# Performance work log

Hardware: AMD Instinct MI355X
Metric: run time of the kernel (lower is better)

Reference implementation:

```python
import jax, jax.numpy as jnp
import numpy as np

B = 32768      # batch
S = 512        # state_dim
G = 128        # goal_dim
A = 32         # action_dim
P = 16         # num_primitives
H1, H2 = 512, 256        # big_model hidden sizes
VH1, VH2 = 1024, 512     # value hidden sizes


def _w(k, shape, scale=0.05):
    return jax.random.normal(k, shape, jnp.float32) * scale


def setup_inputs() -> dict:
    key = jax.random.key(0)
    ks = jax.random.split(key, 24)
    d = {"features": jax.random.normal(ks[0], (B, S + G), jnp.float32)}
    # state encoder: S->H1->H2
    d["se_w1"] = _w(ks[1], (S, H1));  d["se_b1"] = jnp.zeros((H1,), jnp.float32)
    d["se_w2"] = _w(ks[2], (H1, H2)); d["se_b2"] = jnp.zeros((H2,), jnp.float32)
    # goal encoder: G->H1->H2
    d["ge_w1"] = _w(ks[3], (G, H1));  d["ge_b1"] = jnp.zeros((H1,), jnp.float32)
    d["ge_w2"] = _w(ks[4], (H1, H2)); d["ge_b2"] = jnp.zeros((H2,), jnp.float32)
    # gate: 2*H2->H2->P (sigmoid)
    d["gt_w1"] = _w(ks[5], (2 * H2, H2)); d["gt_b1"] = jnp.zeros((H2,), jnp.float32)
    d["gt_w2"] = _w(ks[6], (H2, P));      d["gt_b2"] = jnp.zeros((P,), jnp.float32)
    # primitive state encoder: S->H1->H2
    d["pse_w1"] = _w(ks[7], (S, H1));  d["pse_b1"] = jnp.zeros((H1,), jnp.float32)
    d["pse_w2"] = _w(ks[8], (H1, H2)); d["pse_b2"] = jnp.zeros((H2,), jnp.float32)
    # P primitives, each H2->H2->2A (stacked for batched GEMM)
    d["pw1"] = _w(ks[9], (P, H2, H2));     d["pb1"] = jnp.zeros((P, H2), jnp.float32)
    d["pw2"] = _w(ks[10], (P, H2, 2 * A)); d["pb2"] = jnp.zeros((P, 2 * A), jnp.float32)
    # value net: (S+G)->VH1->VH2
    d["vf_w1"] = _w(ks[11], (S + G, VH1)); d["vf_b1"] = jnp.zeros((VH1,), jnp.float32)
    d["vf_w2"] = _w(ks[12], (VH1, VH2));   d["vf_b2"] = jnp.zeros((VH2,), jnp.float32)
    return d


def _mlp2(x, w1, b1, w2, b2):
    return jax.nn.relu(jax.nn.relu(x @ w1 + b1) @ w2 + b2)


def reference(features,
              se_w1, se_b1, se_w2, se_b2,
              ge_w1, ge_b1, ge_w2, ge_b2,
              gt_w1, gt_b1, gt_w2, gt_b2,
              pse_w1, pse_b1, pse_w2, pse_b2,
              pw1, pb1, pw2, pb2,
              vf_w1, vf_b1, vf_w2, vf_b2):
    state, goal = features[:, :S], features[:, S:]
    # gating weights
    s_emb = _mlp2(state, se_w1, se_b1, se_w2, se_b2)      # [B,H2]
    g_emb = _mlp2(goal, ge_w1, ge_b1, ge_w2, ge_b2)       # [B,H2]
    gate_in = jnp.concatenate([s_emb, g_emb], axis=-1)    # [B,2*H2]
    weights = jax.nn.sigmoid(jax.nn.relu(gate_in @ gt_w1 + gt_b1) @ gt_w2 + gt_b2)  # [B,P]
    # shared primitive embedding
    prim_embed = _mlp2(state, pse_w1, pse_b1, pse_w2, pse_b2)  # [B,H2]
    # all primitives as one batched GEMM
    h = jax.nn.relu(jnp.einsum('bh,phk->bpk', prim_embed, pw1) + pb1[None])  # [B,P,H2]
    out = jnp.einsum('bpk,pkd->bpd', h, pw2) + pb2[None]                      # [B,P,2A]
    mu, log_std = out[..., :A], out[..., A:]
    sigma = jnp.exp(log_std)
    # precision-weighted Gaussian mixture
    inv = weights[..., None] / sigma        # [B,P,A]
    denom = inv.sum(axis=1)                 # [B,A]
    mean = (inv * mu).sum(axis=1) / denom   # [B,A]  (learn_log_std=True -> mean only)
    # critic
    value = _mlp2(features, vf_w1, vf_b1, vf_w2, vf_b2)  # [B,VH2]
    return (mean, value)
```

## Files before the change

kernel.cpp:

```cpp
#include <hip/hip_runtime.h>
#include <stdint.h>

#define NB 32768

typedef __bf16 bf16x8 __attribute__((ext_vector_type(8)));
typedef float f32x4 __attribute__((ext_vector_type(4)));

__device__ __forceinline__ unsigned short f2bf(float f) {
  union { float f; unsigned u; } v; v.f = f;
  unsigned r = v.u + 0x7fffu + ((v.u >> 16) & 1u);
  return (unsigned short)(r >> 16);
}
__device__ __forceinline__ float bf2f(unsigned short h) {
  union { unsigned u; float f; } v; v.u = ((unsigned)h) << 16;
  return v.f;
}

__device__ __forceinline__ void gld_lds16(void* lds, const void* g) {
  __builtin_amdgcn_global_load_lds(
      (__attribute__((address_space(1))) unsigned int*)(uintptr_t)g,
      (__attribute__((address_space(3))) unsigned int*)(uintptr_t)lds,
      16, 0, 0);
}


__global__ __launch_bounds__(256) void fconv_k(const float* __restrict__ src,
                                               unsigned short* __restrict__ dst) {
  size_t idx = ((size_t)blockIdx.x * 256 + threadIdx.x) * 8;
  float4 a = *(const float4*)(src + idx);
  float4 b = *(const float4*)(src + idx + 4);
  union { unsigned short us[8]; uint4 v; } u;
  u.us[0] = f2bf(a.x); u.us[1] = f2bf(a.y); u.us[2] = f2bf(a.z); u.us[3] = f2bf(a.w);
  u.us[4] = f2bf(b.x); u.us[5] = f2bf(b.y); u.us[6] = f2bf(b.z); u.us[7] = f2bf(b.w);
  *(uint4*)(dst + idx) = u.v;
}

struct TJobs {
  const float* src[11];
  unsigned short* dst[11];
  int K[11], N[11], batch[11];
};

__global__ __launch_bounds__(256) void wtrans_k(TJobs jobs) {
  const int job = blockIdx.y;
  const int K = jobs.K[job], N = jobs.N[job];
  const int KT = K >> 5, NT = N >> 5;
  const int ntiles = jobs.batch[job] * KT * NT;
  const int t = blockIdx.x;
  if (t >= ntiles) return;
  const int b = t / (KT * NT);
  const int rem = t - b * KT * NT;
  const int kt = rem / NT, nt = rem - kt * NT;
  const float* src = jobs.src[job] + (size_t)b * K * N;
  unsigned short* dst = jobs.dst[job] + (size_t)b * K * N;
  __shared__ float tile[32][33];
  const int i = threadIdx.x >> 5, jj = threadIdx.x & 31;
#pragma unroll
  for (int s = 0; s < 4; ++s)
    tile[i + 8 * s][jj] = src[(size_t)(kt * 32 + i + 8 * s) * N + nt * 32 + jj];
  __syncthreads();
#pragma unroll
  for (int s = 0; s < 4; ++s)
    dst[(size_t)(nt * 32 + i + 8 * s) * K + kt * 32 + jj] = f2bf(tile[jj][i + 8 * s]);
}


template <bool OUT_BF16>
__global__ __launch_bounds__(256) void gemm_k(const unsigned short* __restrict__ A, int lda,
                                              const unsigned short* __restrict__ WT,
                                              const float* __restrict__ bias,
                                              void* __restrict__ Cout, int ldc, int K) {
  __shared__ unsigned short lds_a[128 * 32];
  __shared__ unsigned short lds_b[128 * 32];
  const int tid = threadIdx.x;
  const int l = tid & 63, w = tid >> 6;
  const int wm = w >> 1, wn = w & 1;
  const int lr = l & 15, lq = l >> 4;
  const int row0 = blockIdx.x << 7;
  const int col0 = blockIdx.y << 7;
  const int srow = tid >> 2;
  const int scg = tid & 3;
  const int wbase = tid & ~63;

  f32x4 acc[4][4] = {};

  for (int k0 = 0; k0 < K; k0 += 32) {
#pragma unroll
    for (int i = 0; i < 2; ++i) {
      const int r = i * 64 + srow;
      gld_lds16(&lds_a[(size_t)(i * 256 + wbase) * 8],
                A + (size_t)(row0 + r) * lda + k0 + scg * 8);
      gld_lds16(&lds_b[(size_t)(i * 256 + wbase) * 8],
                WT + (size_t)(col0 + r) * K + k0 + scg * 8);
    }
    __syncthreads();
    bf16x8 av[4], bv[4];
#pragma unroll
    for (int mf = 0; mf < 4; ++mf)
      av[mf] = *(const bf16x8*)&lds_a[((wm * 64 + mf * 16 + lr) << 5) + (lq << 3)];
#pragma unroll
    for (int nf = 0; nf < 4; ++nf)
      bv[nf] = *(const bf16x8*)&lds_b[((wn * 64 + nf * 16 + lr) << 5) + (lq << 3)];
#pragma unroll
    for (int mf = 0; mf < 4; ++mf)
#pragma unroll
      for (int nf = 0; nf < 4; ++nf)
        acc[mf][nf] = __builtin_amdgcn_mfma_f32_16x16x32_bf16(av[mf], bv[nf], acc[mf][nf], 0, 0, 0);
    __syncthreads();
  }

#pragma unroll
  for (int nf = 0; nf < 4; ++nf) {
    const int gc = col0 + wn * 64 + nf * 16 + lr;
    const float bb = bias[gc];
#pragma unroll
    for (int mf = 0; mf < 4; ++mf) {
      const int gr = row0 + wm * 64 + mf * 16 + (lq << 2);
#pragma unroll
      for (int r = 0; r < 4; ++r) {
        float v = acc[mf][nf][r] + bb;
        v = fmaxf(v, 0.0f);
        if (OUT_BF16)
          ((unsigned short*)Cout)[(size_t)(gr + r) * ldc + gc] = f2bf(v);
        else
          ((float*)Cout)[(size_t)(gr + r) * ldc + gc] = v;
      }
    }
  }
}


template <bool OUT_BF16>
__global__ __launch_bounds__(256, 2) void gemm2_k(const unsigned short* __restrict__ A, int lda,
                                                  const unsigned short* __restrict__ WT,
                                                  const float* __restrict__ bias,
                                                  void* __restrict__ Cout, int ldc, int K) {
  __shared__ unsigned short a_s[2][128 * 32];
  __shared__ unsigned short b_s[2][256 * 32];
  const int tid = threadIdx.x;
  const int l = tid & 63, w = tid >> 6;
  const int lr = l & 15, lq = l >> 4;
  const int row0 = blockIdx.x << 7;
  const int col0 = blockIdx.y << 8;
  const int wbase = tid & ~63;

  auto stage = [&](int buf, int t) {
    const int k0 = t << 5;
#pragma unroll
    for (int i = 0; i < 2; ++i) {
      const int s = i * 256 + tid;
      const int r = s >> 2, c = s & 3;
      const int cs = c ^ ((r >> 1) & 3);
      gld_lds16(&a_s[buf][(size_t)(i * 256 + wbase) * 8],
                A + (size_t)(row0 + r) * lda + k0 + cs * 8);
    }
#pragma unroll
    for (int i = 0; i < 4; ++i) {
      const int s = i * 256 + tid;
      const int n = s >> 2, c = s & 3;
      const int cs = c ^ ((n >> 1) & 3);
      gld_lds16(&b_s[buf][(size_t)(i * 256 + wbase) * 8],
                WT + (size_t)(col0 + n) * K + k0 + cs * 8);
    }
  };

  f32x4 acc[8][4] = {};
  const int nt = K >> 5;
  stage(0, 0);
  __syncthreads();
#pragma unroll 1
  for (int t = 0; t < nt; ++t) {
    const int cur = t & 1;
    if (t + 1 < nt) stage(cur ^ 1, t + 1);
    bf16x8 av[8], bv[4];
#pragma unroll
    for (int mf = 0; mf < 8; ++mf) {
      const int r = mf * 16 + lr;
      av[mf] = *(const bf16x8*)&a_s[cur][r * 32 + ((lq ^ ((r >> 1) & 3)) << 3)];
    }
#pragma unroll
    for (int nf = 0; nf < 4; ++nf) {
      const int n = w * 64 + nf * 16 + lr;
      bv[nf] = *(const bf16x8*)&b_s[cur][n * 32 + ((lq ^ ((n >> 1) & 3)) << 3)];
    }
#pragma unroll
    for (int mf = 0; mf < 8; ++mf)
#pragma unroll
      for (int nf = 0; nf < 4; ++nf)
        acc[mf][nf] = __builtin_amdgcn_mfma_f32_16x16x32_bf16(av[mf], bv[nf], acc[mf][nf], 0, 0, 0);
    __syncthreads();
  }

#pragma unroll
  for (int nf = 0; nf < 4; ++nf) {
    const int gc = col0 + w * 64 + nf * 16 + lr;
    const float bb = bias[gc];
#pragma unroll
    for (int mf = 0; mf < 8; ++mf) {
      const int gr = row0 + mf * 16 + (lq << 2);
#pragma unroll
      for (int r = 0; r < 4; ++r) {
        float v = acc[mf][nf][r] + bb;
        v = fmaxf(v, 0.0f);
        if (OUT_BF16)
          ((unsigned short*)Cout)[(size_t)(gr + r) * ldc + gc] = f2bf(v);
        else
          ((float*)Cout)[(size_t)(gr + r) * ldc + gc] = v;
      }
    }
  }
}


__global__ __launch_bounds__(256) void gt2_k(const unsigned short* __restrict__ gate_h,
                                             const float* __restrict__ w2,
                                             const float* __restrict__ b2,
                                             float* __restrict__ wgt) {
  __shared__ float w_s[256 * 16];
  __shared__ unsigned short a_s[16 * 264];
  const int tid = threadIdx.x;
  const int row0 = blockIdx.x * 16;
  for (int i = tid; i < 256 * 16; i += 256) w_s[i] = w2[i];
  for (int i = tid; i < 512; i += 256) {
    const int r = i >> 5, cg = i & 31;
    *(uint4*)&a_s[r * 264 + cg * 8] =
        *(const uint4*)(gate_h + (size_t)(row0 + r) * 256 + cg * 8);
  }
  __syncthreads();
  const int rr = tid >> 4, col = tid & 15;
  float sum = b2[col];
#pragma unroll 8
  for (int k = 0; k < 256; ++k)
    sum += bf2f(a_s[rr * 264 + k]) * w_s[k * 16 + col];
  wgt[(size_t)(row0 + rr) * 16 + col] = 1.0f / (1.0f + __expf(-sum));
}


__global__ __launch_bounds__(512, 4) void prim_head_k(
    const unsigned short* __restrict__ prim,
    const float* __restrict__ wgt,
    const unsigned short* __restrict__ pw1t,
    const float* __restrict__ pb1,
    const unsigned short* __restrict__ pw2t,
    const float* __restrict__ pb2,
    unsigned short* __restrict__ outbuf)
{
  __shared__ unsigned short prim_s[2][128 * 32];
  __shared__ unsigned short w1_s[2][128 * 32];
  __shared__ unsigned short h_s[128 * 128];
  __shared__ unsigned short pw2_s[64 * 128];
  const int tid = threadIdx.x;
  const int l = tid & 63;
  const int w = tid >> 6;
  const int lr = l & 15, lq = l >> 4;
  const int wn2 = w & 1, wr2 = w >> 1;
  const int row0 = blockIdx.x << 7;
  const int p = blockIdx.y;
  const int wbase = tid & ~63;

  const unsigned short* w1p = pw1t + (size_t)p * 65536;
  const unsigned short* w2p = pw2t + (size_t)p * 16384;

  auto stage_ab = [&](int t) {
    const int buf = t & 1;
    const int k0 = (t & 7) << 5;
    const int nb2 = (t >> 3) << 7;
    const int rw = tid >> 2, kc = tid & 3;
    const int kcs = kc ^ ((rw >> 1) & 3);
    gld_lds16(&prim_s[buf][(size_t)wbase * 8],
              prim + (size_t)(row0 + rw) * 256 + k0 + kcs * 8);
    gld_lds16(&w1_s[buf][(size_t)wbase * 8],
              w1p + (size_t)(nb2 + rw) * 256 + k0 + kcs * 8);
  };
  auto stage_pw2 = [&](int half) {
    const int nbase = half << 7;
#pragma unroll
    for (int i = 0; i < 2; ++i) {
      const int c = i * 512 + tid;
      const int d = c >> 4, kc = c & 15;
      gld_lds16(&pw2_s[(size_t)(i * 512 + wbase) * 8],
                w2p + (size_t)d * 256 + nbase + ((kc ^ (d & 7)) << 3));
    }
  };

  stage_ab(0);
  stage_pw2(0);
  __syncthreads();

  f32x4 acc2[2][2] = {};

  for (int half = 0; half < 2; ++half) {
    float4 pb1v[4];
#pragma unroll
    for (int nf = 0; nf < 4; ++nf)
      pb1v[nf] = *(const float4*)(pb1 + p * 256 + (half << 7) + wn2 * 64 + nf * 16 + (lq << 2));

    f32x4 acc1[4][2] = {};
#pragma unroll 1
    for (int ks = 0; ks < 8; ++ks) {
      const int t = (half << 3) + ks;
      const int cur = t & 1;
      if (t < 15) stage_ab(t + 1);
      bf16x8 av[4], bv[2];
#pragma unroll
      for (int nf = 0; nf < 4; ++nf) {
        const int n = wn2 * 64 + nf * 16 + lr;
        av[nf] = *(const bf16x8*)&w1_s[cur][n * 32 + ((lq ^ ((n >> 1) & 3)) << 3)];
      }
#pragma unroll
      for (int rf = 0; rf < 2; ++rf) {
        const int r = wr2 * 32 + rf * 16 + lr;
        bv[rf] = *(const bf16x8*)&prim_s[cur][r * 32 + ((lq ^ ((r >> 1) & 3)) << 3)];
      }
#pragma unroll
      for (int nf = 0; nf < 4; ++nf)
#pragma unroll
        for (int rf = 0; rf < 2; ++rf)
          acc1[nf][rf] = __builtin_amdgcn_mfma_f32_16x16x32_bf16(av[nf], bv[rf], acc1[nf][rf], 0, 0, 0);
      __syncthreads();
    }

#pragma unroll
    for (int nf = 0; nf < 4; ++nf) {
      const int n0 = wn2 * 64 + nf * 16 + (lq << 2);
      const float4 bb = pb1v[nf];
#pragma unroll
      for (int rf = 0; rf < 2; ++rf) {
        const int row = wr2 * 32 + rf * 16 + lr;
        const float v0 = fmaxf(acc1[nf][rf][0] + bb.x, 0.0f);
        const float v1 = fmaxf(acc1[nf][rf][1] + bb.y, 0.0f);
        const float v2 = fmaxf(acc1[nf][rf][2] + bb.z, 0.0f);
        const float v3 = fmaxf(acc1[nf][rf][3] + bb.w, 0.0f);
        uint2 pk;
        pk.x = (unsigned)f2bf(v0) | ((unsigned)f2bf(v1) << 16);
        pk.y = (unsigned)f2bf(v2) | ((unsigned)f2bf(v3) << 16);
        *(uint2*)&h_s[row * 128 + (((n0 >> 3) ^ (row & 7)) << 3) + (n0 & 7)] = pk;
      }
    }
    __syncthreads();

    {
      const int dmu = wn2 * 16;
      const int row_a = wr2 * 32;
#pragma unroll
      for (int kc8 = 0; kc8 < 4; ++kc8) {
        const int slot = ((kc8 << 2) + lq) ^ (lr & 7);
        const bf16x8 amu = *(const bf16x8*)&pw2_s[(dmu + lr) * 128 + (slot << 3)];
        const bf16x8 als = *(const bf16x8*)&pw2_s[(dmu + 32 + lr) * 128 + (slot << 3)];
        const bf16x8 b0 = *(const bf16x8*)&h_s[(row_a + lr) * 128 + (slot << 3)];
        const bf16x8 b1 = *(const bf16x8*)&h_s[(row_a + 16 + lr) * 128 + (slot << 3)];
        acc2[0][0] = __builtin_amdgcn_mfma_f32_16x16x32_bf16(amu, b0, acc2[0][0], 0, 0, 0);
        acc2[0][1] = __builtin_amdgcn_mfma_f32_16x16x32_bf16(als, b0, acc2[0][1], 0, 0, 0);
        acc2[1][0] = __builtin_amdgcn_mfma_f32_16x16x32_bf16(amu, b1, acc2[1][0], 0, 0, 0);
        acc2[1][1] = __builtin_amdgcn_mfma_f32_16x16x32_bf16(als, b1, acc2[1][1], 0, 0, 0);
      }
    }
    __syncthreads();
    if (half == 0) stage_pw2(1);
  }

  {
    const int dmu = wn2 * 16;
    const int row_a = wr2 * 32;
    const int d0 = dmu + (lq << 2);
    const float4 b2mu = *(const float4*)(pb2 + p * 64 + d0);
    const float4 b2ls = *(const float4*)(pb2 + p * 64 + 32 + d0);
    const float wp0 = wgt[(size_t)(row0 + row_a + lr) * 16 + p];
    const float wp1 = wgt[(size_t)(row0 + row_a + 16 + lr) * 16 + p];
#pragma unroll
    for (int s = 0; s < 2; ++s) {
      const int row_g = row0 + row_a + s * 16 + lr;
      const float wp = s ? wp1 : wp0;
      unsigned short* ob = outbuf + ((size_t)row_g * 16 + p) * 64;
      const float mu0 = acc2[s][0][0] + b2mu.x, ls0 = acc2[s][1][0] + b2ls.x;
      const float mu1 = acc2[s][0][1] + b2mu.y, ls1 = acc2[s][1][1] + b2ls.y;
      const float mu2 = acc2[s][0][2] + b2mu.z, ls2 = acc2[s][1][2] + b2ls.z;
      const float mu3 = acc2[s][0][3] + b2mu.w, ls3 = acc2[s][1][3] + b2ls.w;
      const float iv0 = wp * __expf(-ls0), iv1 = wp * __expf(-ls1);
      const float iv2 = wp * __expf(-ls2), iv3 = wp * __expf(-ls3);
      uint2 nmp, ivp;
      nmp.x = (unsigned)f2bf(iv0 * mu0) | ((unsigned)f2bf(iv1 * mu1) << 16);
      nmp.y = (unsigned)f2bf(iv2 * mu2) | ((unsigned)f2bf(iv3 * mu3) << 16);
      ivp.x = (unsigned)f2bf(iv0) | ((unsigned)f2bf(iv1) << 16);
      ivp.y = (unsigned)f2bf(iv2) | ((unsigned)f2bf(iv3) << 16);
      *(uint2*)(ob + d0) = nmp;
      *(uint2*)(ob + 32 + d0) = ivp;
    }
  }
}


__global__ __launch_bounds__(256) void mix_finish_k(const unsigned short* __restrict__ buf,
                                                    float* __restrict__ mean_out) {
  const int gid = blockIdx.x * 256 + threadIdx.x;
  const int row = gid >> 3;
  const int a0 = (gid & 7) * 4;
  const unsigned short* rp = buf + (size_t)row * 1024;
  float nx = 0, ny = 0, nz = 0, nw = 0, dx = 0, dy = 0, dz = 0, dw = 0;
#pragma unroll
  for (int p = 0; p < 16; ++p) {
    const uint2 m = *(const uint2*)(rp + p * 64 + a0);
    const uint2 v = *(const uint2*)(rp + p * 64 + 32 + a0);
    nx += bf2f((unsigned short)(m.x & 0xffff)); ny += bf2f((unsigned short)(m.x >> 16));
    nz += bf2f((unsigned short)(m.y & 0xffff)); nw += bf2f((unsigned short)(m.y >> 16));
    dx += bf2f((unsigned short)(v.x & 0xffff)); dy += bf2f((unsigned short)(v.x >> 16));
    dz += bf2f((unsigned short)(v.y & 0xffff)); dw += bf2f((unsigned short)(v.y >> 16));
  }
  float4 res;
  res.x = nx / dx; res.y = ny / dy; res.z = nz / dz; res.w = nw / dw;
  *(float4*)(mean_out + (size_t)row * 32 + a0) = res;
}


extern "C" void kernel_launch(void* const* d_in, const int* in_sizes, int n_in,
                              void* d_out, int out_size, void* d_ws, size_t ws_size,
                              hipStream_t stream) {
  const float* features = (const float*)d_in[0];
  const float* se_w1 = (const float*)d_in[1];
  const float* se_b1 = (const float*)d_in[2];
  const float* se_w2 = (const float*)d_in[3];
  const float* se_b2 = (const float*)d_in[4];
  const float* ge_w1 = (const float*)d_in[5];
  const float* ge_b1 = (const float*)d_in[6];
  const float* ge_w2 = (const float*)d_in[7];
  const float* ge_b2 = (const float*)d_in[8];
  const float* gt_w1 = (const float*)d_in[9];
  const float* gt_b1 = (const float*)d_in[10];
  const float* gt_w2 = (const float*)d_in[11];
  const float* gt_b2 = (const float*)d_in[12];
  const float* pse_w1 = (const float*)d_in[13];
  const float* pse_b1 = (const float*)d_in[14];
  const float* pse_w2 = (const float*)d_in[15];
  const float* pse_b2 = (const float*)d_in[16];
  const float* pw1 = (const float*)d_in[17];
  const float* pb1 = (const float*)d_in[18];
  const float* pw2 = (const float*)d_in[19];
  const float* pb2 = (const float*)d_in[20];
  const float* vf_w1 = (const float*)d_in[21];
  const float* vf_b1 = (const float*)d_in[22];
  const float* vf_w2 = (const float*)d_in[23];
  const float* vf_b2 = (const float*)d_in[24];
  (void)in_sizes; (void)n_in; (void)out_size; (void)ws_size;

  char* base = (char*)d_ws;
  size_t off = 0;
  auto alloc = [&](size_t bytes) -> char* {
    char* p = base + off;
    off += (bytes + 255) & ~(size_t)255;
    return p;
  };
  unsigned short* fbf     = (unsigned short*)alloc((size_t)NB * 640 * 2);
  unsigned short* bufA    = (unsigned short*)alloc((size_t)NB * 1024 * 2);
  unsigned short* g1      = (unsigned short*)alloc((size_t)NB * 512 * 2);
  unsigned short* gate_in = (unsigned short*)alloc((size_t)NB * 512 * 2);
  unsigned short* gate_h  = (unsigned short*)alloc((size_t)NB * 256 * 2);
  unsigned short* prim    = (unsigned short*)alloc((size_t)NB * 256 * 2);
  float* wgt              = (float*)alloc((size_t)NB * 16 * 4);
  unsigned short* se_w1t  = (unsigned short*)alloc(512 * 512 * 2);
  unsigned short* se_w2t  = (unsigned short*)alloc(256 * 512 * 2);
  unsigned short* ge_w1t  = (unsigned short*)alloc(512 * 128 * 2);
  unsigned short* ge_w2t  = (unsigned short*)alloc(256 * 512 * 2);
  unsigned short* gt_w1t  = (unsigned short*)alloc(256 * 512 * 2);
  unsigned short* pse_w1t = (unsigned short*)alloc(512 * 512 * 2);
  unsigned short* pse_w2t = (unsigned short*)alloc(256 * 512 * 2);
  unsigned short* pw1t    = (unsigned short*)alloc((size_t)16 * 256 * 256 * 2);
  unsigned short* pw2t    = (unsigned short*)alloc((size_t)16 * 64 * 256 * 2);
  unsigned short* vf_w1t  = (unsigned short*)alloc(1024 * 640 * 2);
  unsigned short* vf_w2t  = (unsigned short*)alloc(512 * 1024 * 2);

  unsigned short* outbuf = (unsigned short*)bufA;

  float* mean_out = (float*)d_out;
  float* value_out = (float*)d_out + (size_t)NB * 32;

  fconv_k<<<dim3(10240), dim3(256), 0, stream>>>(features, fbf);

  TJobs jobs;
  auto setj = [&](int i, const float* s, unsigned short* d, int K, int N, int b) {
    jobs.src[i] = s; jobs.dst[i] = d; jobs.K[i] = K; jobs.N[i] = N; jobs.batch[i] = b;
  };
  setj(0, se_w1, se_w1t, 512, 512, 1);
  setj(1, se_w2, se_w2t, 512, 256, 1);
  setj(2, ge_w1, ge_w1t, 128, 512, 1);
  setj(3, ge_w2, ge_w2t, 512, 256, 1);
  setj(4, gt_w1, gt_w1t, 512, 256, 1);
  setj(5, pse_w1, pse_w1t, 512, 512, 1);
  setj(6, pse_w2, pse_w2t, 512, 256, 1);
  setj(7, pw1, pw1t, 256, 256, 16);
  setj(8, pw2, pw2t, 256, 64, 16);
  setj(9, vf_w1, vf_w1t, 640, 1024, 1);
  setj(10, vf_w2, vf_w2t, 1024, 512, 1);
  wtrans_k<<<dim3(1024, 11), dim3(256), 0, stream>>>(jobs);

  gemm2_k<true><<<dim3(256, 2), dim3(256), 0, stream>>>(fbf, 640, se_w1t, se_b1, bufA, 512, 512);
  gemm_k<true><<<dim3(256, 2), dim3(256), 0, stream>>>(bufA, 512, se_w2t, se_b2, gate_in, 512, 512);
  gemm2_k<true><<<dim3(256, 2), dim3(256), 0, stream>>>(fbf + 512, 640, ge_w1t, ge_b1, g1, 512, 128);
  gemm_k<true><<<dim3(256, 2), dim3(256), 0, stream>>>(g1, 512, ge_w2t, ge_b2, gate_in + 256, 512, 512);
  gemm_k<true><<<dim3(256, 2), dim3(256), 0, stream>>>(gate_in, 512, gt_w1t, gt_b1, gate_h, 256, 512);
  gt2_k<<<dim3(2048), dim3(256), 0, stream>>>(gate_h, gt_w2, gt_b2, wgt);
  gemm2_k<true><<<dim3(256, 2), dim3(256), 0, stream>>>(fbf, 640, pse_w1t, pse_b1, bufA, 512, 512);
  gemm_k<true><<<dim3(256, 2), dim3(256), 0, stream>>>(bufA, 512, pse_w2t, pse_b2, prim, 256, 512);
  gemm2_k<true><<<dim3(256, 4), dim3(256), 0, stream>>>(fbf, 640, vf_w1t, vf_b1, bufA, 1024, 640);
  gemm2_k<false><<<dim3(256, 2), dim3(256), 0, stream>>>(bufA, 1024, vf_w2t, vf_b2, value_out, 512, 1024);
  prim_head_k<<<dim3(256, 16), dim3(512), 0, stream>>>(prim, wgt, pw1t, pb1, pw2t, pb2, outbuf);
  mix_finish_k<<<dim3(1024), dim3(256), 0, stream>>>(outbuf, mean_out);
}
```

Before: 478.8 us.

## Replace single-buffered GEMM with double-buffered swizzled kernel and XCD-aware tile mapping

Replaces the old single-buffered 128x128 gemm_k with a new gemm3_k. The new kernel double-buffers its LDS tiles so the next K-slice loads while the current one computes, and uses an XOR swizzle to reduce LDS bank conflicts. Both GEMM kernels now take a 1D grid and remap block ids so consecutive tiles land on the same XCD, which improves L2 reuse of A rows across column tiles. The cost is more LDS per block and extra index arithmetic, and the grid sizes must stay divisible by 8.

```diff
diff --git a/kernel.cpp b/kernel.cpp
--- a/kernel.cpp
+++ b/kernel.cpp
@@ -21,6 +21,10 @@
       (__attribute__((address_space(1))) unsigned int*)(uintptr_t)g,
       (__attribute__((address_space(3))) unsigned int*)(uintptr_t)lds,
       16, 0, 0);
+}
+
+__device__ __forceinline__ int xcd_swz(int bid, int nwg) {
+  return (bid & 7) * (nwg >> 3) + (bid >> 3);
 }
 
 
@@ -66,82 +70,19 @@
 
 
 template <bool OUT_BF16>
-__global__ __launch_bounds__(256) void gemm_k(const unsigned short* __restrict__ A, int lda,
-                                              const unsigned short* __restrict__ WT,
-                                              const float* __restrict__ bias,
-                                              void* __restrict__ Cout, int ldc, int K) {
-  __shared__ unsigned short lds_a[128 * 32];
-  __shared__ unsigned short lds_b[128 * 32];
-  const int tid = threadIdx.x;
-  const int l = tid & 63, w = tid >> 6;
-  const int wm = w >> 1, wn = w & 1;
-  const int lr = l & 15, lq = l >> 4;
-  const int row0 = blockIdx.x << 7;
-  const int col0 = blockIdx.y << 7;
-  const int srow = tid >> 2;
-  const int scg = tid & 3;
-  const int wbase = tid & ~63;
-
-  f32x4 acc[4][4] = {};
-
-  for (int k0 = 0; k0 < K; k0 += 32) {
-#pragma unroll
-    for (int i = 0; i < 2; ++i) {
-      const int r = i * 64 + srow;
-      gld_lds16(&lds_a[(size_t)(i * 256 + wbase) * 8],
-                A + (size_t)(row0 + r) * lda + k0 + scg * 8);
-      gld_lds16(&lds_b[(size_t)(i * 256 + wbase) * 8],
-                WT + (size_t)(col0 + r) * K + k0 + scg * 8);
-    }
-    __syncthreads();
-    bf16x8 av[4], bv[4];
-#pragma unroll
-    for (int mf = 0; mf < 4; ++mf)
-      av[mf] = *(const bf16x8*)&lds_a[((wm * 64 + mf * 16 + lr) << 5) + (lq << 3)];
-#pragma unroll
-    for (int nf = 0; nf < 4; ++nf)
-      bv[nf] = *(const bf16x8*)&lds_b[((wn * 64 + nf * 16 + lr) << 5) + (lq << 3)];
-#pragma unroll
-    for (int mf = 0; mf < 4; ++mf)
-#pragma unroll
-      for (int nf = 0; nf < 4; ++nf)
-        acc[mf][nf] = __builtin_amdgcn_mfma_f32_16x16x32_bf16(av[mf], bv[nf], acc[mf][nf], 0, 0, 0);
-    __syncthreads();
-  }
-
-#pragma unroll
-  for (int nf = 0; nf < 4; ++nf) {
-    const int gc = col0 + wn * 64 + nf * 16 + lr;
-    const float bb = bias[gc];
-#pragma unroll
-    for (int mf = 0; mf < 4; ++mf) {
-      const int gr = row0 + wm * 64 + mf * 16 + (lq << 2);
-#pragma unroll
-      for (int r = 0; r < 4; ++r) {
-        float v = acc[mf][nf][r] + bb;
-        v = fmaxf(v, 0.0f);
-        if (OUT_BF16)
-          ((unsigned short*)Cout)[(size_t)(gr + r) * ldc + gc] = f2bf(v);
-        else
-          ((float*)Cout)[(size_t)(gr + r) * ldc + gc] = v;
-      }
-    }
-  }
-}
-
-
-template <bool OUT_BF16>
 __global__ __launch_bounds__(256, 2) void gemm2_k(const unsigned short* __restrict__ A, int lda,
                                                   const unsigned short* __restrict__ WT,
                                                   const float* __restrict__ bias,
-                                                  void* __restrict__ Cout, int ldc, int K) {
+                                                  void* __restrict__ Cout, int ldc, int K,
+                                                  int ncl2) {
   __shared__ unsigned short a_s[2][128 * 32];
   __shared__ unsigned short b_s[2][256 * 32];
   const int tid = threadIdx.x;
   const int l = tid & 63, w = tid >> 6;
   const int lr = l & 15, lq = l >> 4;
-  const int row0 = blockIdx.x << 7;
-  const int col0 = blockIdx.y << 8;
+  const int wg = xcd_swz(blockIdx.x, gridDim.x);
+  const int col0 = (wg & ((1 << ncl2) - 1)) << 8;
+  const int row0 = (wg >> ncl2) << 7;
   const int wbase = tid & ~63;
 
   auto stage = [&](int buf, int t) {
@@ -198,6 +139,91 @@
 #pragma unroll
     for (int mf = 0; mf < 8; ++mf) {
       const int gr = row0 + mf * 16 + (lq << 2);
+#pragma unroll
+      for (int r = 0; r < 4; ++r) {
+        float v = acc[mf][nf][r] + bb;
+        v = fmaxf(v, 0.0f);
+        if (OUT_BF16)
+          ((unsigned short*)Cout)[(size_t)(gr + r) * ldc + gc] = f2bf(v);
+        else
+          ((float*)Cout)[(size_t)(gr + r) * ldc + gc] = v;
+      }
+    }
+  }
+}
+
+
+template <bool OUT_BF16>
+__global__ __launch_bounds__(256, 2) void gemm3_k(const unsigned short* __restrict__ A, int lda,
+                                                  const unsigned short* __restrict__ WT,
+                                                  const float* __restrict__ bias,
+                                                  void* __restrict__ Cout, int ldc, int K,
+                                                  int ncl2) {
+  __shared__ unsigned short a_s[2][128 * 32];
+  __shared__ unsigned short b_s[2][128 * 32];
+  const int tid = threadIdx.x;
+  const int l = tid & 63, w = tid >> 6;
+  const int wm = w >> 1, wn = w & 1;
+  const int lr = l & 15, lq = l >> 4;
+  const int wg = xcd_swz(blockIdx.x, gridDim.x);
+  const int col0 = (wg & ((1 << ncl2) - 1)) << 7;
+  const int row0 = (wg >> ncl2) << 7;
+  const int wbase = tid & ~63;
+
+  auto stage = [&](int buf, int t) {
+    const int k0 = t << 5;
+#pragma unroll
+    for (int i = 0; i < 2; ++i) {
+      const int s = i * 256 + tid;
+      const int r = s >> 2, c = s & 3;
+      const int cs = c ^ ((r >> 1) & 3);
+      gld_lds16(&a_s[buf][(size_t)(i * 256 + wbase) * 8],
+                A + (size_t)(row0 + r) * lda + k0 + cs * 8);
+    }
+#pragma unroll
+    for (int i = 0; i < 2; ++i) {
+      const int s = i * 256 + tid;
+      const int n = s >> 2, c = s & 3;
+      const int cs = c ^ ((n >> 1) & 3);
+      gld_lds16(&b_s[buf][(size_t)(i * 256 + wbase) * 8],
+                WT + (size_t)(col0 + n) * K + k0 + cs * 8);
+    }
+  };
+
+  f32x4 acc[4][4] = {};
+  const int nt = K >> 5;
+  stage(0, 0);
+  __syncthreads();
+#pragma unroll 1
+  for (int t = 0; t < nt; ++t) {
+    const int cur = t & 1;
+    if (t + 1 < nt) stage(cur ^ 1, t + 1);
+    bf16x8 av[4], bv[4];
+#pragma unroll
+    for (int mf = 0; mf < 4; ++mf) {
+      const int r = wm * 64 + mf * 16 + lr;
+      av[mf] = *(const bf16x8*)&a_s[cur][r * 32 + ((lq ^ ((r >> 1) & 3)) << 3)];
+    }
+#pragma unroll
+    for (int nf = 0; nf < 4; ++nf) {
+      const int n = wn * 64 + nf * 16 + lr;
+      bv[nf] = *(const bf16x8*)&b_s[cur][n * 32 + ((lq ^ ((n >> 1) & 3)) << 3)];
+    }
+#pragma unroll
+    for (int mf = 0; mf < 4; ++mf)
+#pragma unroll
+      for (int nf = 0; nf < 4; ++nf)
+        acc[mf][nf] = __builtin_amdgcn_mfma_f32_16x16x32_bf16(av[mf], bv[nf], acc[mf][nf], 0, 0, 0);
+    __syncthreads();
+  }
+
+#pragma unroll
+  for (int nf = 0; nf < 4; ++nf) {
+    const int gc = col0 + wn * 64 + nf * 16 + lr;
+    const float bb = bias[gc];
+#pragma unroll
+    for (int mf = 0; mf < 4; ++mf) {
+      const int gr = row0 + wm * 64 + mf * 16 + (lq << 2);
 #pragma unroll
       for (int r = 0; r < 4; ++r) {
         float v = acc[mf][nf][r] + bb;
@@ -492,16 +518,16 @@
   setj(10, vf_w2, vf_w2t, 1024, 512, 1);
   wtrans_k<<<dim3(1024, 11), dim3(256), 0, stream>>>(jobs);
 
-  gemm2_k<true><<<dim3(256, 2), dim3(256), 0, stream>>>(fbf, 640, se_w1t, se_b1, bufA, 512, 512);
-  gemm_k<true><<<dim3(256, 2), dim3(256), 0, stream>>>(bufA, 512, se_w2t, se_b2, gate_in, 512, 512);
-  gemm2_k<true><<<dim3(256, 2), dim3(256), 0, stream>>>(fbf + 512, 640, ge_w1t, ge_b1, g1, 512, 128);
-  gemm_k<true><<<dim3(256, 2), dim3(256), 0, stream>>>(g1, 512, ge_w2t, ge_b2, gate_in + 256, 512, 512);
-  gemm_k<true><<<dim3(256, 2), dim3(256), 0, stream>>>(gate_in, 512, gt_w1t, gt_b1, gate_h, 256, 512);
+  gemm2_k<true><<<dim3(512), dim3(256), 0, stream>>>(fbf, 640, se_w1t, se_b1, bufA, 512, 512, 1);
+  gemm3_k<true><<<dim3(512), dim3(256), 0, stream>>>(bufA, 512, se_w2t, se_b2, gate_in, 512, 512, 1);
+  gemm2_k<true><<<dim3(512), dim3(256), 0, stream>>>(fbf + 512, 640, ge_w1t, ge_b1, g1, 512, 128, 1);
+  gemm3_k<true><<<dim3(512), dim3(256), 0, stream>>>(g1, 512, ge_w2t, ge_b2, gate_in + 256, 512, 512, 1);
+  gemm3_k<true><<<dim3(512), dim3(256), 0, stream>>>(gate_in, 512, gt_w1t, gt_b1, gate_h, 256, 512, 1);
   gt2_k<<<dim3(2048), dim3(256), 0, stream>>>(gate_h, gt_w2, gt_b2, wgt);
-  gemm2_k<true><<<dim3(256, 2), dim3(256), 0, stream>>>(fbf, 640, pse_w1t, pse_b1, bufA, 512, 512);
-  gemm_k<true><<<dim3(256, 2), dim3(256), 0, stream>>>(bufA, 512, pse_w2t, pse_b2, prim, 256, 512);
-  gemm2_k<true><<<dim3(256, 4), dim3(256), 0, stream>>>(fbf, 640, vf_w1t, vf_b1, bufA, 1024, 640);
-  gemm2_k<false><<<dim3(256, 2), dim3(256), 0, stream>>>(bufA, 1024, vf_w2t, vf_b2, value_out, 512, 1024);
+  gemm2_k<true><<<dim3(512), dim3(256), 0, stream>>>(fbf, 640, pse_w1t, pse_b1, bufA, 512, 512, 1);
+  gemm3_k<true><<<dim3(512), dim3(256), 0, stream>>>(bufA, 512, pse_w2t, pse_b2, prim, 256, 512, 1);
+  gemm2_k<true><<<dim3(1024), dim3(256), 0, stream>>>(fbf, 640, vf_w1t, vf_b1, bufA, 1024, 640, 2);
+  gemm2_k<false><<<dim3(512), dim3(256), 0, stream>>>(bufA, 1024, vf_w2t, vf_b2, value_out, 512, 1024, 1);
   prim_head_k<<<dim3(256, 16), dim3(512), 0, stream>>>(prim, wgt, pw1t, pb1, pw2t, pb2, outbuf);
   mix_finish_k<<<dim3(1024), dim3(256), 0, stream>>>(outbuf, mean_out);
 }
```

New measurement: 457.3 us. 4.5% less time.
